# Kernel optimization log

Measured on AMD Instinct MI355X. Metric: run time of the kernel, lower is better.

Reference implementation:

```python
import jax, jax.numpy as jnp
import numpy as np

DIM = 256
NUM_HEADS = 8
HEAD_DIM = DIM // NUM_HEADS


def setup_inputs() -> dict:
    key = jax.random.key(0)
    k_x, k_wq, k_bq, k_wp, k_bp = jax.random.split(key, 5)
    B, C, H, W = 2, DIM, 48, 48
    x = jax.random.normal(k_x, (B, C, H, W), dtype=jnp.float32)
    # 1x1 convs are pointwise matmuls: store weights as [out, in]
    w_qkv = jax.random.normal(k_wq, (3 * C, C), dtype=jnp.float32) * (1.0 / np.sqrt(C))
    b_qkv = jax.random.normal(k_bq, (3 * C,), dtype=jnp.float32) * 0.01
    w_proj = jax.random.normal(k_wp, (C, C), dtype=jnp.float32) * (1.0 / np.sqrt(C))
    b_proj = jax.random.normal(k_bp, (C,), dtype=jnp.float32) * 0.01
    return {"x": x, "w_qkv": w_qkv, "b_qkv": b_qkv, "w_proj": w_proj, "b_proj": b_proj}


def reference(x, w_qkv, b_qkv, w_proj, b_proj):
    B, C, H, W = x.shape
    N = H * W
    # qkv 1x1 conv -> pointwise channel matmul
    qkv = jnp.einsum('bchw,oc->bohw', x, w_qkv) + b_qkv[None, :, None, None]
    q, k, v = jnp.split(qkv, 3, axis=1)  # each [B, C, H, W]
    q = q.reshape(B, NUM_HEADS, HEAD_DIM, N)
    k = k.reshape(B, NUM_HEADS, HEAD_DIM, N)
    v = v.reshape(B, NUM_HEADS, HEAD_DIM, N)
    scale = 1.0 / (HEAD_DIM ** 0.5)
    attn = jnp.einsum('bhdn,bhdm->bhnm', q, k) * scale  # [B, H, N, N]
    attn = jax.nn.softmax(attn, axis=-1)
    out = jnp.einsum('bhnm,bhdm->bhdn', attn, v)  # [B, heads, head_dim, N]
    out = out.reshape(B, C, H, W)
    out = jnp.einsum('bchw,oc->bohw', out, w_proj) + b_proj[None, :, None, None]
    return out + x
```

## Files before the change

### kernel.cpp

```cpp
#include <hip/hip_runtime.h>
#include <math.h>

#define C_DIM 256
#define NH 8
#define HD 32
#define BATCH 2
#define NPIX 2304
#define TK 64
#define NGRP (NPIX / 16)
#define TPB 18

typedef __attribute__((ext_vector_type(8))) short bf16x8;
typedef __attribute__((ext_vector_type(4))) float f32x4;

#define OFF_XT  0u
#define OFF_Q   1179648u
#define OFF_K   2359296u
#define OFF_V   3538944u
#define OFF_OT  4718592u
#define OFF_WQ  5898240u
#define OFF_WP  6094848u
#define OFF_F32 6160384u

__device__ __forceinline__ unsigned short f2b(float f) {
    union { float f; unsigned int u; } c; c.f = f;
    unsigned int u = c.u + 0x7FFFu + ((c.u >> 16) & 1u);
    return (unsigned short)(u >> 16);
}
__device__ __forceinline__ unsigned int pk2(float lo, float hi) {
    union { float f; unsigned int u; } a, b;
    a.f = lo; b.f = hi;
    return __builtin_amdgcn_perm(b.u + 0x8000u, a.u + 0x8000u, 0x07060302u);
}

__global__ __launch_bounds__(256) void prep_xt(
        const float* __restrict__ x, unsigned short* __restrict__ xT)
{
    __shared__ unsigned short t_s[64][72];
    const int tid = threadIdx.x;
    const int n0 = blockIdx.x * 64, c0 = blockIdx.y * 64, b = blockIdx.z;
    const int nl = tid & 63, cq = tid >> 6;
    #pragma unroll
    for (int p = 0; p < 8; ++p) {
        const int c = p * 8 + cq * 2;
        const float f0 = x[((size_t)b * C_DIM + c0 + c) * NPIX + n0 + nl];
        const float f1 = x[((size_t)b * C_DIM + c0 + c + 1) * NPIX + n0 + nl];
        *(unsigned int*)&t_s[nl][c] = pk2(f0, f1);
    }
    __syncthreads();
    const int row = tid >> 2, jq = tid & 3;
    #pragma unroll
    for (int hh = 0; hh < 2; ++hh) {
        const int jl = jq * 2 + hh;
        const int jg = blockIdx.y * 8 + jl;
        const int ngrp = blockIdx.x * 4 + (row >> 4);
        unsigned short* dst = xT + (((size_t)b * NGRP + ngrp) * 32 + jg) * 128 + (row & 15) * 8;
        *(uint4*)dst = *(uint4*)&t_s[row][jl * 8];
    }
}

__global__ __launch_bounds__(256) void prep_w(
        const float* __restrict__ wqkv, const float* __restrict__ wproj,
        unsigned short* __restrict__ wq, unsigned short* __restrict__ wp)
{
    const int t = blockIdx.x * 256 + threadIdx.x;
    const float* src; unsigned short* dst;
    if (t < 24576) {
        const int m = t >> 5, j = t & 31;
        src = wqkv + ((size_t)m * C_DIM + j * 8);
        dst = wq + ((size_t)((m >> 4) * 32 + j) * 16 + (m & 15)) * 8;
    } else {
        const int t2 = t - 24576, m = t2 >> 5, j = t2 & 31;
        src = wproj + ((size_t)m * C_DIM + j * 8);
        dst = wp + ((size_t)((m >> 4) * 32 + j) * 16 + (m & 15)) * 8;
    }
    const float4 f0 = *(const float4*)src, f1 = *(const float4*)(src + 4);
    *(uint4*)dst = make_uint4(pk2(f0.x, f0.y), pk2(f0.z, f0.w),
                              pk2(f1.x, f1.y), pk2(f1.z, f1.w));
}

__global__ __launch_bounds__(256, 2) void qkv_gemm(
        const unsigned short* __restrict__ xT, const unsigned short* __restrict__ wq,
        const float* __restrict__ bias,
        unsigned short* __restrict__ Qg, unsigned short* __restrict__ Kg,
        unsigned short* __restrict__ Vg)
{
    __shared__ unsigned short eplds[4][2560];
    const int tid = threadIdx.x, wv = tid >> 6, lane = tid & 63;
    const int l15 = lane & 15, quad = lane >> 4;
    const int n0 = blockIdx.x * 256, my = blockIdx.y, b = blockIdx.z;
    const int nw = n0 + wv * 64;

    bf16x8 af[2][8];
    #pragma unroll
    for (int mt = 0; mt < 2; ++mt)
        #pragma unroll
        for (int kc = 0; kc < 8; ++kc)
            af[mt][kc] = *(const bf16x8*)(wq +
                ((size_t)((my * 2 + mt) * 32 + kc * 4 + quad) * 16 + l15) * 8);

    f32x4 acc[2][4];
    #pragma unroll
    for (int mt = 0; mt < 2; ++mt)
        #pragma unroll
        for (int s = 0; s < 4; ++s) acc[mt][s] = (f32x4){0.f, 0.f, 0.f, 0.f};

    #pragma unroll
    for (int sub = 0; sub < 4; ++sub) {
        const int ngrp = (nw + sub * 16) >> 4;
        const unsigned short* bp = xT + ((size_t)b * NGRP + ngrp) * 32 * 128;
        #pragma unroll
        for (int kc = 0; kc < 8; ++kc) {
            const bf16x8 bf = *(const bf16x8*)(bp + (size_t)(kc * 4 + quad) * 128 + l15 * 8);
            acc[0][sub] = __builtin_amdgcn_mfma_f32_16x16x32_bf16(af[0][kc], bf, acc[0][sub], 0, 0, 0);
            acc[1][sub] = __builtin_amdgcn_mfma_f32_16x16x32_bf16(af[1][kc], bf, acc[1][sub], 0, 0, 0);
        }
    }

    const int which = my >> 3;
    const int h = my & 7, bh = b * NH + h;
    float4 b4[2];
    b4[0] = *(const float4*)(bias + my * 32 + quad * 4);
    b4[1] = *(const float4*)(bias + my * 32 + 16 + quad * 4);
    unsigned short* wl = eplds[wv];

    if (which < 2) {
        const float sc = (which == 0) ? 0.17677669529663687f : 1.0f;
        #pragma unroll
        for (int mt = 0; mt < 2; ++mt)
            #pragma unroll
            for (int sub = 0; sub < 4; ++sub) {
                const float v0 = (acc[mt][sub][0] + b4[mt].x) * sc;
                const float v1 = (acc[mt][sub][1] + b4[mt].y) * sc;
                const float v2 = (acc[mt][sub][2] + b4[mt].z) * sc;
                const float v3 = (acc[mt][sub][3] + b4[mt].w) * sc;
                *(uint2*)&wl[(sub * 16 + l15) * 40 + mt * 16 + quad * 4] =
                    make_uint2(pk2(v0, v1), pk2(v2, v3));
            }
        unsigned short* dst = ((which == 0) ? Qg : Kg)
                            + ((size_t)bh * NPIX + nw + lane) * HD;
        #pragma unroll
        for (int i = 0; i < 4; ++i)
            *((uint4*)dst + i) = *(uint4*)&wl[lane * 40 + i * 8];
    } else {
        #pragma unroll
        for (int mt = 0; mt < 2; ++mt)
            #pragma unroll
            for (int sub = 0; sub < 4; ++sub) {
                wl[(mt * 16 + quad * 4 + 0) * 72 + sub * 16 + l15] = f2b(acc[mt][sub][0] + b4[mt].x);
                wl[(mt * 16 + quad * 4 + 1) * 72 + sub * 16 + l15] = f2b(acc[mt][sub][1] + b4[mt].y);
                wl[(mt * 16 + quad * 4 + 2) * 72 + sub * 16 + l15] = f2b(acc[mt][sub][2] + b4[mt].z);
                wl[(mt * 16 + quad * 4 + 3) * 72 + sub * 16 + l15] = f2b(acc[mt][sub][3] + b4[mt].w);
            }
        const int row = lane >> 1, seg = (lane & 1) * 32;
        unsigned short* dst = Vg + ((size_t)bh * HD + row) * NPIX + nw + seg;
        #pragma unroll
        for (int i = 0; i < 4; ++i)
            *((uint4*)dst + i) = *(uint4*)&wl[row * 72 + seg + i * 8];
    }
}

__global__ __launch_bounds__(256, 4) void attn_kernel(
        const unsigned short* __restrict__ Qg, const unsigned short* __restrict__ Kg,
        const unsigned short* __restrict__ Vg,
        float* __restrict__ OtP, float* __restrict__ lsumP)
{
    __shared__ unsigned short k_s[2][TK][40];
    __shared__ unsigned short v_s[2][HD][76];
    __shared__ unsigned short p_s[4][16][76];

    const int tid  = threadIdx.x;
    const int wv   = tid >> 6;
    const int lane = tid & 63;
    const int l15  = lane & 15;
    const int quad = lane >> 4;
    const int bh   = blockIdx.x;
    const int q0   = blockIdx.y * 64;
    const int sp   = blockIdx.z;
    const int t0   = sp * TPB;

    const unsigned short* Qh = Qg + (size_t)bh * NPIX * HD;
    const unsigned short* Kh = Kg + (size_t)bh * NPIX * HD;
    const unsigned short* Vh = Vg + (size_t)bh * HD * NPIX;

    const bf16x8 q_frag = *(const bf16x8*)(Qh + (size_t)(q0 + wv * 16 + l15) * HD + quad * 8);

    const int kr = tid >> 2, kc = (tid & 3) * 8;
    const int vd = tid >> 3, vc = (tid & 7) * 8;

    uint4 kreg = *(const uint4*)(Kh + (size_t)(t0 * TK + kr) * HD + kc);
    uint4 vreg = *(const uint4*)(Vh + (size_t)vd * NPIX + t0 * TK + vc);
    *(uint4*)&k_s[0][kr][kc] = kreg;
    *(uint4*)&v_s[0][vd][vc] = vreg;

    f32x4 o0 = {0.f, 0.f, 0.f, 0.f};
    f32x4 o1 = {0.f, 0.f, 0.f, 0.f};
    float lsum = 0.f;

    for (int t = 0; t < TPB; ++t) {
        const int cur = t & 1;
        if (t + 1 < TPB) {
            const int k0 = (t0 + t + 1) * TK;
            kreg = *(const uint4*)(Kh + (size_t)(k0 + kr) * HD + kc);
            vreg = *(const uint4*)(Vh + (size_t)vd * NPIX + k0 + vc);
        }
        __syncthreads();

        f32x4 s[4];
        #pragma unroll
        for (int kg = 0; kg < 4; ++kg) {
            const bf16x8 kf = *(const bf16x8*)&k_s[cur][kg * 16 + l15][quad * 8];
            s[kg] = __builtin_amdgcn_mfma_f32_16x16x32_bf16(kf, q_frag,
                        (f32x4){0.f, 0.f, 0.f, 0.f}, 0, 0, 0);
        }

        #pragma unroll
        for (int kg = 0; kg < 4; ++kg) {
            const float p0 = __expf(s[kg][0]);
            const float p1 = __expf(s[kg][1]);
            const float p2 = __expf(s[kg][2]);
            const float p3 = __expf(s[kg][3]);
            lsum += (p0 + p1) + (p2 + p3);
            *(uint2*)&p_s[wv][l15][kg * 16 + quad * 4] =
                make_uint2(pk2(p0, p1), pk2(p2, p3));
        }

        #pragma unroll
        for (int kc2 = 0; kc2 < 2; ++kc2) {
            const bf16x8 pf  = *(const bf16x8*)&p_s[wv][l15][kc2 * 32 + quad * 8];
            const bf16x8 vf0 = *(const bf16x8*)&v_s[cur][l15][kc2 * 32 + quad * 8];
            const bf16x8 vf1 = *(const bf16x8*)&v_s[cur][16 + l15][kc2 * 32 + quad * 8];
            o0 = __builtin_amdgcn_mfma_f32_16x16x32_bf16(vf0, pf, o0, 0, 0, 0);
            o1 = __builtin_amdgcn_mfma_f32_16x16x32_bf16(vf1, pf, o1, 0, 0, 0);
        }

        if (t + 1 < TPB) {
            *(uint4*)&k_s[cur ^ 1][kr][kc] = kreg;
            *(uint4*)&v_s[cur ^ 1][vd][vc] = vreg;
        }
    }

    lsum += __shfl_xor(lsum, 16, 64);
    lsum += __shfl_xor(lsum, 32, 64);

    __syncthreads();
    float* pp = (float*)&p_s[wv][0][0];
    #pragma unroll
    for (int r = 0; r < 4; ++r) {
        pp[l15 * 36 + quad * 4 + r]      = o0[r];
        pp[l15 * 36 + 16 + quad * 4 + r] = o1[r];
    }
    if (quad == 0)
        lsumP[((size_t)sp * 16 + bh) * NPIX + q0 + wv * 16 + l15] = lsum;
    __syncthreads();
    const int q = lane >> 2, off = (lane & 3) * 8;
    float* dst = OtP + (((size_t)sp * 16 + bh) * NPIX + q0 + wv * 16 + q) * 32 + off;
    *(float4*)dst       = *(float4*)&pp[q * 36 + off];
    *((float4*)dst + 1) = *(float4*)&pp[q * 36 + off + 4];
}

__global__ __launch_bounds__(256) void norm_kernel(
        const float* __restrict__ OtP, const float* __restrict__ lsumP,
        unsigned short* __restrict__ OtT)
{
    const int q = blockIdx.x * 256 + threadIdx.x;
    const int bh = blockIdx.y;
    const float* pa = OtP + ((size_t)bh * NPIX + q) * 32;
    const float* pb = OtP + ((size_t)(16 + bh) * NPIX + q) * 32;
    const float inv = 1.f / (lsumP[(size_t)bh * NPIX + q] +
                             lsumP[(size_t)(16 + bh) * NPIX + q]);
    const int b = bh >> 3, h = bh & 7;
    unsigned short* cell = OtT + (((size_t)b * NGRP + (q >> 4)) * 32 + h * 4) * 128
                         + (q & 15) * 8;
    #pragma unroll
    for (int jq = 0; jq < 4; ++jq) {
        const float4 a0 = *(const float4*)(pa + jq * 8);
        const float4 a1 = *(const float4*)(pa + jq * 8 + 4);
        const float4 b0 = *(const float4*)(pb + jq * 8);
        const float4 b1 = *(const float4*)(pb + jq * 8 + 4);
        const float o0 = (a0.x + b0.x) * inv, o1 = (a0.y + b0.y) * inv;
        const float o2 = (a0.z + b0.z) * inv, o3 = (a0.w + b0.w) * inv;
        const float o4 = (a1.x + b1.x) * inv, o5 = (a1.y + b1.y) * inv;
        const float o6 = (a1.z + b1.z) * inv, o7 = (a1.w + b1.w) * inv;
        *(uint4*)(cell + jq * 128) = make_uint4(pk2(o0, o1), pk2(o2, o3),
                                                pk2(o4, o5), pk2(o6, o7));
    }
}

__global__ __launch_bounds__(256) void proj_gemm(
        const unsigned short* __restrict__ OtT, const unsigned short* __restrict__ wp,
        const float* __restrict__ bias, const float* __restrict__ x,
        float* __restrict__ out)
{
    __shared__ float plds[4][576];
    const int tid = threadIdx.x, wv = tid >> 6, lane = tid & 63;
    const int l15 = lane & 15, quad = lane >> 4;
    const int n0 = blockIdx.x * 128, my = blockIdx.y, b = blockIdx.z;
    const int nw = n0 + wv * 32;

    bf16x8 af[8];
    #pragma unroll
    for (int kc = 0; kc < 8; ++kc)
        af[kc] = *(const bf16x8*)(wp + ((size_t)(my * 32 + kc * 4 + quad) * 16 + l15) * 8);

    f32x4 acc[2];
    acc[0] = (f32x4){0.f, 0.f, 0.f, 0.f};
    acc[1] = (f32x4){0.f, 0.f, 0.f, 0.f};

    #pragma unroll
    for (int sub = 0; sub < 2; ++sub) {
        const int ngrp = (nw + sub * 16) >> 4;
        const unsigned short* bp = OtT + ((size_t)b * NGRP + ngrp) * 32 * 128;
        #pragma unroll
        for (int kc = 0; kc < 8; ++kc) {
            const bf16x8 bf = *(const bf16x8*)(bp + (size_t)(kc * 4 + quad) * 128 + l15 * 8);
            acc[sub] = __builtin_amdgcn_mfma_f32_16x16x32_bf16(af[kc], bf, acc[sub], 0, 0, 0);
        }
    }

    float* wl = plds[wv];
    #pragma unroll
    for (int sub = 0; sub < 2; ++sub) {
        wl[(quad * 4 + 0) * 36 + sub * 16 + l15] = acc[sub][0];
        wl[(quad * 4 + 1) * 36 + sub * 16 + l15] = acc[sub][1];
        wl[(quad * 4 + 2) * 36 + sub * 16 + l15] = acc[sub][2];
        wl[(quad * 4 + 3) * 36 + sub * 16 + l15] = acc[sub][3];
    }
    const int m0 = my * 16;
    #pragma unroll
    for (int p = 0; p < 2; ++p) {
        const int row = p * 8 + (lane >> 3), cn = (lane & 7) * 4;
        const int c = m0 + row;
        const size_t idx = ((size_t)b * C_DIM + c) * NPIX + nw + cn;
        const f32x4 v = *(const f32x4*)&wl[row * 36 + cn];
        const f32x4 r = *(const f32x4*)(x + idx);
        const float bv = bias[c];
        f32x4 o;
        o[0] = v[0] + bv + r[0]; o[1] = v[1] + bv + r[1];
        o[2] = v[2] + bv + r[2]; o[3] = v[3] + bv + r[3];
        *(f32x4*)(out + idx) = o;
    }
}

extern "C" void kernel_launch(void* const* d_in, const int* in_sizes, int n_in,
                              void* d_out, int out_size, void* d_ws, size_t ws_size,
                              hipStream_t stream)
{
    const float* x      = (const float*)d_in[0];
    const float* w_qkv  = (const float*)d_in[1];
    const float* b_qkv  = (const float*)d_in[2];
    const float* w_proj = (const float*)d_in[3];
    const float* b_proj = (const float*)d_in[4];
    float* out = (float*)d_out;

    unsigned short* ws = (unsigned short*)d_ws;
    unsigned short* xT  = ws + OFF_XT;
    unsigned short* Qg  = ws + OFF_Q;
    unsigned short* Kg  = ws + OFF_K;
    unsigned short* Vg  = ws + OFF_V;
    unsigned short* OtT = ws + OFF_OT;
    unsigned short* wq  = ws + OFF_WQ;
    unsigned short* wp  = ws + OFF_WP;
    float* fws   = (float*)(ws + OFF_F32);
    float* OtP   = fws;
    float* lsumP = fws + 4718592;

    prep_xt<<<dim3(36, 4, 2), 256, 0, stream>>>(x, xT);
    prep_w<<<dim3(128), 256, 0, stream>>>(w_qkv, w_proj, wq, wp);
    qkv_gemm<<<dim3(9, 24, 2), 256, 0, stream>>>(xT, wq, b_qkv, Qg, Kg, Vg);
    attn_kernel<<<dim3(16, 36, 2), 256, 0, stream>>>(Qg, Kg, Vg, OtP, lsumP);
    norm_kernel<<<dim3(9, 16), 256, 0, stream>>>(OtP, lsumP, OtT);
    proj_gemm<<<dim3(18, 16, 2), 256, 0, stream>>>(OtT, wp, b_proj, x, out);
}
```

Baseline: 117.9 us.

## Merge prep kernels into one launch and use exp2 with log2e-folded Q scale

Combines the x-transpose and weight-conversion prep kernels into a single launch with a flat grid, removing one kernel launch. The Q scale now includes log2(e) so the attention kernel can use exp2f instead of __expf. The norm kernel grid axes are swapped, and a __syncthreads is added in proj_gemm before reading the LDS staging. The extra barrier adds a small cost but may fix a cross-lane race.

```diff
diff --git a/kernel.cpp b/kernel.cpp
--- a/kernel.cpp
+++ b/kernel.cpp
@@ -4,10 +4,9 @@
 #define C_DIM 256
 #define NH 8
 #define HD 32
-#define BATCH 2
 #define NPIX 2304
+#define NGRP 144
 #define TK 64
-#define NGRP (NPIX / 16)
 #define TPB 18
 
 typedef __attribute__((ext_vector_type(8))) short bf16x8;
@@ -33,50 +32,51 @@
     return __builtin_amdgcn_perm(b.u + 0x8000u, a.u + 0x8000u, 0x07060302u);
 }
 
-__global__ __launch_bounds__(256) void prep_xt(
-        const float* __restrict__ x, unsigned short* __restrict__ xT)
+__global__ __launch_bounds__(256) void prep_all(
+        const float* __restrict__ x, const float* __restrict__ wqkv,
+        const float* __restrict__ wproj, unsigned short* __restrict__ wsp)
 {
     __shared__ unsigned short t_s[64][72];
     const int tid = threadIdx.x;
-    const int n0 = blockIdx.x * 64, c0 = blockIdx.y * 64, b = blockIdx.z;
-    const int nl = tid & 63, cq = tid >> 6;
-    #pragma unroll
-    for (int p = 0; p < 8; ++p) {
-        const int c = p * 8 + cq * 2;
-        const float f0 = x[((size_t)b * C_DIM + c0 + c) * NPIX + n0 + nl];
-        const float f1 = x[((size_t)b * C_DIM + c0 + c + 1) * NPIX + n0 + nl];
-        *(unsigned int*)&t_s[nl][c] = pk2(f0, f1);
-    }
-    __syncthreads();
-    const int row = tid >> 2, jq = tid & 3;
-    #pragma unroll
-    for (int hh = 0; hh < 2; ++hh) {
-        const int jl = jq * 2 + hh;
-        const int jg = blockIdx.y * 8 + jl;
-        const int ngrp = blockIdx.x * 4 + (row >> 4);
-        unsigned short* dst = xT + (((size_t)b * NGRP + ngrp) * 32 + jg) * 128 + (row & 15) * 8;
-        *(uint4*)dst = *(uint4*)&t_s[row][jl * 8];
-    }
-}
-
-__global__ __launch_bounds__(256) void prep_w(
-        const float* __restrict__ wqkv, const float* __restrict__ wproj,
-        unsigned short* __restrict__ wq, unsigned short* __restrict__ wp)
-{
-    const int t = blockIdx.x * 256 + threadIdx.x;
-    const float* src; unsigned short* dst;
-    if (t < 24576) {
-        const int m = t >> 5, j = t & 31;
-        src = wqkv + ((size_t)m * C_DIM + j * 8);
-        dst = wq + ((size_t)((m >> 4) * 32 + j) * 16 + (m & 15)) * 8;
+    const int u = blockIdx.x;
+    if (u < 288) {
+        const int n0 = (u % 36) * 64, cb = (u / 36) % 4, b = u / 144;
+        const int c0 = cb * 64;
+        const int nl = tid & 63, cq = tid >> 6;
+        #pragma unroll
+        for (int p = 0; p < 8; ++p) {
+            const int c = p * 8 + cq * 2;
+            const float f0 = x[((size_t)b * C_DIM + c0 + c) * NPIX + n0 + nl];
+            const float f1 = x[((size_t)b * C_DIM + c0 + c + 1) * NPIX + n0 + nl];
+            *(unsigned int*)&t_s[nl][c] = pk2(f0, f1);
+        }
+        __syncthreads();
+        unsigned short* xT = wsp + OFF_XT;
+        const int row = tid >> 2, jq = tid & 3;
+        #pragma unroll
+        for (int hh = 0; hh < 2; ++hh) {
+            const int jl = jq * 2 + hh;
+            const int jg = cb * 8 + jl;
+            const int ngrp = (u % 36) * 4 + (row >> 4);
+            unsigned short* dst = xT + (((size_t)b * NGRP + ngrp) * 32 + jg) * 128 + (row & 15) * 8;
+            *(uint4*)dst = *(uint4*)&t_s[row][jl * 8];
+        }
     } else {
-        const int t2 = t - 24576, m = t2 >> 5, j = t2 & 31;
-        src = wproj + ((size_t)m * C_DIM + j * 8);
-        dst = wp + ((size_t)((m >> 4) * 32 + j) * 16 + (m & 15)) * 8;
-    }
-    const float4 f0 = *(const float4*)src, f1 = *(const float4*)(src + 4);
-    *(uint4*)dst = make_uint4(pk2(f0.x, f0.y), pk2(f0.z, f0.w),
-                              pk2(f1.x, f1.y), pk2(f1.z, f1.w));
+        const int t = (u - 288) * 256 + tid;
+        const float* src; unsigned short* dst;
+        if (t < 24576) {
+            const int m = t >> 5, j = t & 31;
+            src = wqkv + ((size_t)m * C_DIM + j * 8);
+            dst = wsp + OFF_WQ + ((size_t)((m >> 4) * 32 + j) * 16 + (m & 15)) * 8;
+        } else {
+            const int t2 = t - 24576, m = t2 >> 5, j = t2 & 31;
+            src = wproj + ((size_t)m * C_DIM + j * 8);
+            dst = wsp + OFF_WP + ((size_t)((m >> 4) * 32 + j) * 16 + (m & 15)) * 8;
+        }
+        const float4 f0 = *(const float4*)src, f1 = *(const float4*)(src + 4);
+        *(uint4*)dst = make_uint4(pk2(f0.x, f0.y), pk2(f0.z, f0.w),
+                                  pk2(f1.x, f1.y), pk2(f1.z, f1.w));
+    }
 }
 
 __global__ __launch_bounds__(256, 2) void qkv_gemm(
@@ -125,7 +125,7 @@
     unsigned short* wl = eplds[wv];
 
     if (which < 2) {
-        const float sc = (which == 0) ? 0.17677669529663687f : 1.0f;
+        const float sc = (which == 0) ? 0.25503484f : 1.0f;
         #pragma unroll
         for (int mt = 0; mt < 2; ++mt)
             #pragma unroll
@@ -216,10 +216,10 @@
 
         #pragma unroll
         for (int kg = 0; kg < 4; ++kg) {
-            const float p0 = __expf(s[kg][0]);
-            const float p1 = __expf(s[kg][1]);
-            const float p2 = __expf(s[kg][2]);
-            const float p3 = __expf(s[kg][3]);
+            const float p0 = exp2f(s[kg][0]);
+            const float p1 = exp2f(s[kg][1]);
+            const float p2 = exp2f(s[kg][2]);
+            const float p3 = exp2f(s[kg][3]);
             lsum += (p0 + p1) + (p2 + p3);
             *(uint2*)&p_s[wv][l15][kg * 16 + quad * 4] =
                 make_uint2(pk2(p0, p1), pk2(p2, p3));
@@ -263,8 +263,8 @@
         const float* __restrict__ OtP, const float* __restrict__ lsumP,
         unsigned short* __restrict__ OtT)
 {
-    const int q = blockIdx.x * 256 + threadIdx.x;
-    const int bh = blockIdx.y;
+    const int bh = blockIdx.x;
+    const int q = blockIdx.y * 256 + threadIdx.x;
     const float* pa = OtP + ((size_t)bh * NPIX + q) * 32;
     const float* pb = OtP + ((size_t)(16 + bh) * NPIX + q) * 32;
     const float inv = 1.f / (lsumP[(size_t)bh * NPIX + q] +
@@ -309,7 +309,7 @@
 
     #pragma unroll
     for (int sub = 0; sub < 2; ++sub) {
-        const int ngrp = (nw + sub * 16) >> 4;
+        const int ngrp = (nw >> 4) + sub;
         const unsigned short* bp = OtT + ((size_t)b * NGRP + ngrp) * 32 * 128;
         #pragma unroll
         for (int kc = 0; kc < 8; ++kc) {
@@ -326,6 +326,7 @@
         wl[(quad * 4 + 2) * 36 + sub * 16 + l15] = acc[sub][2];
         wl[(quad * 4 + 3) * 36 + sub * 16 + l15] = acc[sub][3];
     }
+    __syncthreads();
     const int m0 = my * 16;
     #pragma unroll
     for (int p = 0; p < 2; ++p) {
@@ -365,10 +366,9 @@
     float* OtP   = fws;
     float* lsumP = fws + 4718592;
 
-    prep_xt<<<dim3(36, 4, 2), 256, 0, stream>>>(x, xT);
-    prep_w<<<dim3(128), 256, 0, stream>>>(w_qkv, w_proj, wq, wp);
+    prep_all<<<dim3(416), 256, 0, stream>>>(x, w_qkv, w_proj, ws);
     qkv_gemm<<<dim3(9, 24, 2), 256, 0, stream>>>(xT, wq, b_qkv, Qg, Kg, Vg);
     attn_kernel<<<dim3(16, 36, 2), 256, 0, stream>>>(Qg, Kg, Vg, OtP, lsumP);
-    norm_kernel<<<dim3(9, 16), 256, 0, stream>>>(OtP, lsumP, OtT);
+    norm_kernel<<<dim3(16, 9), 256, 0, stream>>>(OtP, lsumP, OtT);
     proj_gemm<<<dim3(18, 16, 2), 256, 0, stream>>>(OtT, wp, b_proj, x, out);
 }
```

Measured after the change: 122.6 us. 4.0% more time.
